# Performance work log

Measured on AMD Instinct MI355X. Metric: run time of the kernel, lower is better.

The kernel has to match this reference:

```python
import jax, jax.numpy as jnp
import numpy as np

B, P, H = 256, 20, 4  # images, boxes per image, humans per image
F, L, S, HD, C = 1024, 300, 16, 1024, 117

def _build_edges():
    s, d = np.meshgrid(np.arange(P), np.arange(P), indexing='ij')
    m = s != d
    src_l, dst_l = s[m], d[m]  # 380 fully-connected edges per image (src-major order)
    eid_tab = -np.ones((P, P), np.int64)
    eid_tab[src_l, dst_l] = np.arange(src_l.shape[0])
    rs, rd = np.meshgrid(np.arange(P), np.arange(H), indexing='ij')
    rm = rs != rd
    r_eid = eid_tab[rs[rm], rd[rm]]  # 76 readout edges per image (human dst)
    off_n = (np.arange(B) * P)[:, None]
    off_e = (np.arange(B) * src_l.shape[0])[:, None]
    edge_src = (src_l[None] + off_n).ravel().astype(np.int32)
    edge_dst = (dst_l[None] + off_n).ravel().astype(np.int32)
    readout_eid = (r_eid[None] + off_e).ravel().astype(np.int32)
    return edge_src, edge_dst, readout_eid

def setup_inputs() -> dict:
    key = jax.random.key(0)
    ks = jax.random.split(key, 12)
    es, ed, re = _build_edges()
    N = B * P
    D_in = 2 * F + 2 * L + S  # 2664
    return {
        'feat': jax.random.normal(ks[0], (N, F), jnp.float32),
        'word2vec': jax.random.normal(ks[1], (N, L), jnp.float32),
        'spatial_feat': jax.random.normal(ks[2], (es.shape[0], S), jnp.float32),
        'W_v': jax.random.normal(ks[3], (F, F), jnp.float32) / np.float32(np.sqrt(F)),
        'a_v': jax.random.normal(ks[4], (2 * F,), jnp.float32) * 0.05,
        'W_l': jax.random.normal(ks[5], (L, L), jnp.float32) / np.float32(np.sqrt(L)),
        'a_l': jax.random.normal(ks[6], (2 * L,), jnp.float32) * 0.05,
        'W1': jax.random.normal(ks[7], (D_in, HD), jnp.float32) / np.float32(np.sqrt(D_in)),
        'b1': jnp.zeros((HD,), jnp.float32),
        'W2': jax.random.normal(ks[8], (HD, C), jnp.float32) / np.float32(np.sqrt(HD)),
        'b2': jnp.zeros((C,), jnp.float32),
        'edge_src': jnp.asarray(es),
        'edge_dst': jnp.asarray(ed),
        'readout_eid': jnp.asarray(re),
    }

def _gat_update(x, W, a, src, dst, n):
    # graph-attention message passing (GRNN step): attention over incoming edges per dst
    h = x @ W                      # [N, d]
    d = h.shape[1]
    e_src = h @ a[:d]              # [N]
    e_dst = h @ a[d:]
    e = jax.nn.leaky_relu(e_src[src] + e_dst[dst], 0.2)          # [E]
    emax = jax.ops.segment_max(e, dst, num_segments=n)
    ee = jnp.exp(e - emax[dst])
    denom = jax.ops.segment_sum(ee, dst, num_segments=n)
    alpha = ee / (denom[dst] + 1e-9)                              # segment softmax
    msg = jax.ops.segment_sum(alpha[:, None] * h[src], dst, num_segments=n)  # [N, d]
    return jax.nn.relu(x + msg)

def reference(feat, word2vec, spatial_feat, W_v, a_v, W_l, a_l, W1, b1, W2, b2,
              edge_src, edge_dst, readout_eid):
    n = feat.shape[0]
    new_n_f = _gat_update(feat, W_v, a_v, edge_src, edge_dst, n)          # visual stream
    new_n_f_lang = _gat_update(word2vec, W_l, a_l, edge_src, edge_dst, n) # semantic stream
    s = edge_src[readout_eid]
    d = edge_dst[readout_eid]
    s_f = spatial_feat[readout_eid]
    # Predictor.forward: concat [dst visual, dst lang, edge spatial, src lang, src visual]
    x = jnp.concatenate([new_n_f[d], new_n_f_lang[d], s_f, new_n_f_lang[s], new_n_f[s]], axis=1)
    hdn = jax.nn.relu(x @ W1 + b1)
    return hdn @ W2 + b2  # [Er, 117] action logits
```

## Files before the change

kernel.cpp:

```cpp
#include <hip/hip_runtime.h>
#include <hip/hip_bf16.h>

#define BB 256
#define PP 20
#define HH 4
#define FF 1024
#define LL 300
#define LLP 320
#define DCAT 1344
#define SS 16
#define HDIM 1024
#define CC 117
#define NNODE (BB * PP)
#define NREAD (BB * (PP * HH - HH))
#define EPB 8
#define TK 32

typedef __attribute__((ext_vector_type(8))) short bf16x8v;
typedef __attribute__((ext_vector_type(4))) float f32x4v;
typedef __attribute__((ext_vector_type(4))) unsigned short u16x4;

__device__ __forceinline__ float bf2f(unsigned short u) {
  return __uint_as_float((unsigned int)u << 16);
}
__device__ __forceinline__ unsigned short f2b(float f) {
  __hip_bfloat16 h = __float2bfloat16(f);
  return *(unsigned short*)&h;
}

__global__ void sniff_dtype(const unsigned short* __restrict__ buf,
                            int* __restrict__ flag) {
  int t = threadIdx.x;
  int votes = 0;
  for (int i = t; i < 512; i += 256) {
    unsigned int u = (unsigned int)buf[i] << 16;
    float v = __uint_as_float(u);
    float a = fabsf(v);
    if (v == v && a > 9.3e-10f && a < 1.1e9f) votes++;
  }
  __shared__ int sv[256];
  sv[t] = votes;
  __syncthreads();
  for (int s = 128; s > 0; s >>= 1) {
    if (t < s) sv[t] += sv[t + s];
    __syncthreads();
  }
  if (t == 0) flag[0] = (sv[0] < 448) ? 1 : 0;
}

#define NB_FEAT 5120
#define NB_W2V 1600
#define NB_SM 79
#define PREP_BLOCKS 10739

__global__ __launch_bounds__(256) void prep_all(
    const void* __restrict__ s0, const void* __restrict__ s1,
    const void* __restrict__ s3, const void* __restrict__ s4,
    const void* __restrict__ s5, const void* __restrict__ s6,
    const void* __restrict__ s7, const void* __restrict__ s8,
    const void* __restrict__ s9, const void* __restrict__ s10,
    __hip_bfloat16* __restrict__ xcat, __hip_bfloat16* __restrict__ cAv,
    __hip_bfloat16* __restrict__ cAl, __hip_bfloat16* __restrict__ cB1,
    __hip_bfloat16* __restrict__ cB2, __hip_bfloat16* __restrict__ cW1sp,
    __hip_bfloat16* __restrict__ dWvT, __hip_bfloat16* __restrict__ dWlT,
    __hip_bfloat16* __restrict__ dW1d, __hip_bfloat16* __restrict__ dW1s,
    __hip_bfloat16* __restrict__ dW2T, const int* __restrict__ flag) {
  const int bid = blockIdx.x;
  const int t = threadIdx.x;
  const int fl = flag[0];

  if (bid < NB_FEAT) {
    long i = (long)bid * 256 + t;
    int r = (int)(i >> 8);
    int c = ((int)i & 255) * 4;
    u16x4 o;
    if (fl) {
      float4 v = *(const float4*)((const float*)s0 + (long)r * FF + c);
      o[0] = f2b(v.x); o[1] = f2b(v.y); o[2] = f2b(v.z); o[3] = f2b(v.w);
    } else {
      o = *(const u16x4*)((const __hip_bfloat16*)s0 + (long)r * FF + c);
    }
    *(u16x4*)(xcat + (long)r * DCAT + c) = o;
  } else if (bid < NB_FEAT + NB_W2V) {
    long i = (long)(bid - NB_FEAT) * 256 + t;
    int r = (int)(i / 80), c = ((int)(i % 80)) * 4;
    u16x4 o;
    if (c + 4 <= LL) {
      if (fl) {
        const float* p = (const float*)s1 + (long)r * LL + c;
        o[0] = f2b(p[0]); o[1] = f2b(p[1]); o[2] = f2b(p[2]); o[3] = f2b(p[3]);
      } else {
        const __hip_bfloat16* p = (const __hip_bfloat16*)s1 + (long)r * LL + c;
        o[0] = *(const unsigned short*)(p + 0);
        o[1] = *(const unsigned short*)(p + 1);
        o[2] = *(const unsigned short*)(p + 2);
        o[3] = *(const unsigned short*)(p + 3);
      }
    } else {
#pragma unroll
      for (int j = 0; j < 4; j++) {
        float v = 0.f;
        if (c + j < LL)
          v = fl ? ((const float*)s1)[(long)r * LL + c + j]
                 : __bfloat162float(
                       ((const __hip_bfloat16*)s1)[(long)r * LL + c + j]);
        o[j] = f2b(v);
      }
    }
    *(u16x4*)(xcat + (long)r * DCAT + FF + c) = o;
  } else if (bid < NB_FEAT + NB_W2V + NB_SM) {
    int i = (bid - NB_FEAT - NB_W2V) * 256 + t;
    auto rd = [&](const void* p, long idx) -> float {
      return fl ? ((const float*)p)[idx]
                : __bfloat162float(((const __hip_bfloat16*)p)[idx]);
    };
    if (i < 2048) cAv[i] = __float2bfloat16(rd(s4, i));
    else if (i < 2648) cAl[i - 2048] = __float2bfloat16(rd(s6, i - 2048));
    else if (i < 3672) cB1[i - 2648] = __float2bfloat16(rd(s8, i - 2648));
    else if (i < 3789) cB2[i - 3672] = __float2bfloat16(rd(s10, i - 3672));
    else if (i < 20173)
      cW1sp[i - 3789] = __float2bfloat16(rd(s7, 1355776L + (i - 3789)));
  } else {
    int idx = bid - (NB_FEAT + NB_W2V + NB_SM);
    const int OFFS[8] = {0, 1024, 1124, 2148, 2468, 3492, 3812, 3940};
    const int NKB[7] = {32, 10, 32, 10, 32, 10, 32};
    const int ROW0[7] = {0, 0, 0, 1024, 1640, 1340, 0};
    const int KK[7] = {1024, 300, 1024, 300, 1024, 300, 1024};
    const int NN[7] = {1024, 300, 1024, 1024, 1024, 1024, 117};
    const int LD[7] = {1024, 300, 1024, 1024, 1024, 1024, 117};
    const int KP[7] = {1024, 320, 1024, 320, 1024, 320, 1024};
    const int KOFF[7] = {0, 0, 0, 1024, 0, 1024, 0};
    const int KLD[7] = {1024, 320, DCAT, DCAT, DCAT, DCAT, 1024};
    int z = 0;
    while (z < 6 && idx >= OFFS[z + 1]) z++;
    idx -= OFFS[z];
    const int kb = (idx % NKB[z]) * 32, nb = (idx / NKB[z]) * 32;
    const void* src = (z == 0) ? s3 : (z == 1) ? s5 : (z == 6) ? s9 : s7;
    __hip_bfloat16* dst = (z == 0) ? dWvT : (z == 1) ? dWlT
                          : (z <= 3) ? dW1d : (z <= 5) ? dW1s : dW2T;
    const int row0 = ROW0[z], K = KK[z], N = NN[z], ld = LD[z], Kp = KP[z];
    const int koff = KOFF[z], kld = KLD[z];
    __shared__ float tile[32][33];
    const int tx = t & 31, ty = t >> 5;
    for (int i = ty; i < 32; i += 8) {
      int k = kb + i, n = nb + tx;
      float v = 0.f;
      if (k < K && n < N) {
        long sidx = (long)(row0 + k) * ld + n;
        v = fl ? ((const float*)src)[sidx]
               : __bfloat162float(((const __hip_bfloat16*)src)[sidx]);
      }
      tile[i][tx] = v;
    }
    __syncthreads();
    for (int i = ty; i < 32; i += 8) {
      int n = nb + i, k = kb + tx;
      if (n < N && k < Kp)
        dst[(long)n * kld + koff + k] = __float2bfloat16(tile[tx][i]);
    }
  }
}

struct GDesc {
  const __hip_bfloat16* A;
  const __hip_bfloat16* BT;
  void* C;
  const __hip_bfloat16* bias;
  int M, N, K, lda, ldbt, ldc;
  int row_mode, do_relu, c_mode, nbx, nby;
};

template <int BM, int BN, int WR, int WC>
__global__ __launch_bounds__(256) void gemm_db(GDesc d0, GDesc d1,
                                               const int* outflag) {
  constexpr int MI = BM / WR / 16;
  constexpr int NI = BN / WC / 16;
  __shared__ __hip_bfloat16 Asm[2][BM * TK];
  __shared__ __hip_bfloat16 Bsm[2][BN * TK];
  const GDesc d = blockIdx.z ? d1 : d0;
  if ((int)blockIdx.x >= d.nbx || (int)blockIdx.y >= d.nby) return;
  const int tid = threadIdx.x;
  const int lane = tid & 63;
  const int wave = tid >> 6;
  const int wm = (wave % WR) * (BM / WR);
  const int wn = (wave / WR) * (BN / WC);
  const int m0 = blockIdx.y * BM;
  const int n0 = blockIdx.x * BN;
  const int col_l = lane & 15;
  const int quad = lane >> 4;
  const __hip_bfloat16* A = d.A;
  const __hip_bfloat16* BT = d.BT;
  const int M = d.M, N = d.N, lda = d.lda, ldbt = d.ldbt;
  const int row_mode = d.row_mode;

  auto stage = [&](int k0, int buf) {
#pragma unroll
    for (int c = tid; c < BM * 4; c += 256) {
      int r = c >> 2;
      int koff = (c & 3) * 8;
      int row = m0 + r;
      if (row >= M) row = M - 1;
      long grow = row_mode ? ((long)(row >> 2) * PP + (row & 3)) : (long)row;
      const __hip_bfloat16* gp = A + grow * lda + k0 + koff;
      __builtin_amdgcn_global_load_lds(
          (const __attribute__((address_space(1))) unsigned int*)gp,
          (__attribute__((address_space(3))) unsigned int*)(&Asm[buf][c * 8]),
          16, 0, 0);
    }
#pragma unroll
    for (int c = tid; c < BN * 4; c += 256) {
      int r = c >> 2;
      int koff = (c & 3) * 8;
      int row = n0 + r;
      if (row >= N) row = N - 1;
      const __hip_bfloat16* gp = BT + (long)row * ldbt + k0 + koff;
      __builtin_amdgcn_global_load_lds(
          (const __attribute__((address_space(1))) unsigned int*)gp,
          (__attribute__((address_space(3))) unsigned int*)(&Bsm[buf][c * 8]),
          16, 0, 0);
    }
  };

  f32x4v acc[MI][NI];
#pragma unroll
  for (int i = 0; i < MI; i++)
#pragma unroll
    for (int j = 0; j < NI; j++)
#pragma unroll
      for (int r = 0; r < 4; r++) acc[i][j][r] = 0.f;

  const int nk = d.K / TK;
  stage(0, 0);
  __syncthreads();
  for (int kt = 0; kt < nk; kt++) {
    const int cur = kt & 1;
    if (kt + 1 < nk) stage((kt + 1) * TK, 1 - cur);
    bf16x8v af[MI], bfr[NI];
#pragma unroll
    for (int mi = 0; mi < MI; mi++)
      af[mi] =
          *(const bf16x8v*)&Asm[cur][(wm + mi * 16 + col_l) * TK + quad * 8];
#pragma unroll
    for (int ni = 0; ni < NI; ni++)
      bfr[ni] =
          *(const bf16x8v*)&Bsm[cur][(wn + ni * 16 + col_l) * TK + quad * 8];
#pragma unroll
    for (int mi = 0; mi < MI; mi++)
#pragma unroll
      for (int ni = 0; ni < NI; ni++)
        acc[mi][ni] = __builtin_amdgcn_mfma_f32_16x16x32_bf16(
            af[mi], bfr[ni], acc[mi][ni], 0, 0, 0);
    __syncthreads();
  }

  const int store_f32 =
      (d.c_mode == 1) || (d.c_mode == 2 && outflag && outflag[0]);
#pragma unroll
  for (int mi = 0; mi < MI; mi++) {
    int rbase = m0 + wm + mi * 16 + quad * 4;
#pragma unroll
    for (int ni = 0; ni < NI; ni++) {
      int col = n0 + wn + ni * 16 + col_l;
      if (col >= N) continue;
      float bv = d.bias ? __bfloat162float(d.bias[col]) : 0.f;
#pragma unroll
      for (int r = 0; r < 4; r++) {
        int row = rbase + r;
        if (row >= M) continue;
        float v = acc[mi][ni][r] + bv;
        if (d.do_relu) v = fmaxf(v, 0.f);
        if (store_f32)
          ((float*)d.C)[(long)row * d.ldc + col] = v;
        else
          ((__hip_bfloat16*)d.C)[(long)row * d.ldc + col] = __float2bfloat16(v);
      }
    }
  }
}

#define CHROW (DCAT / 4)

__global__ __launch_bounds__(1024) void attn_fused(
    const __hip_bfloat16* __restrict__ xcat,
    const __hip_bfloat16* __restrict__ hcat,
    const __hip_bfloat16* __restrict__ aV,
    const __hip_bfloat16* __restrict__ aL,
    __hip_bfloat16* __restrict__ newcat) {
  const int b = blockIdx.x;
  const int t = threadIdx.x;
  const long base = (long)b * PP * DCAT;

  __shared__ __hip_bfloat16 hs[PP][DCAT];
  __shared__ float esv[PP], edv[PP], esl[PP], edl[PP];
  __shared__ float alphaV[PP * PP], alphaL[PP * PP];

  for (int i = t; i < PP * CHROW; i += 1024) {
    int r = i / CHROW, c = (i % CHROW) * 4;
    *(u16x4*)&hs[r][c] = *(const u16x4*)(hcat + base + (long)r * DCAT + c);
  }
  __syncthreads();

  const int wave = t >> 6, lane = t & 63;
  for (int node = wave; node < PP; node += 16) {
    float s1 = 0.f, s2 = 0.f, s3 = 0.f, s4 = 0.f;
    for (int f = lane * 4; f < FF; f += 256) {
      u16x4 hv = *(const u16x4*)&hs[node][f];
      u16x4 a1 = *(const u16x4*)(aV + f);
      u16x4 a2 = *(const u16x4*)(aV + FF + f);
#pragma unroll
      for (int j = 0; j < 4; j++) {
        float hf = bf2f(hv[j]);
        s1 += hf * bf2f(a1[j]);
        s2 += hf * bf2f(a2[j]);
      }
    }
    for (int f = FF + lane * 4; f < FF + LL; f += 256) {
      u16x4 hv = *(const u16x4*)&hs[node][f];
      u16x4 a3 = *(const u16x4*)(aL + (f - FF));
      u16x4 a4 = *(const u16x4*)(aL + LL + (f - FF));
#pragma unroll
      for (int j = 0; j < 4; j++) {
        float hf = bf2f(hv[j]);
        s3 += hf * bf2f(a3[j]);
        s4 += hf * bf2f(a4[j]);
      }
    }
#pragma unroll
    for (int o = 32; o > 0; o >>= 1) {
      s1 += __shfl_down(s1, o);
      s2 += __shfl_down(s2, o);
      s3 += __shfl_down(s3, o);
      s4 += __shfl_down(s4, o);
    }
    if (lane == 0) {
      esv[node] = s1; edv[node] = s2; esl[node] = s3; edl[node] = s4;
    }
  }
  __syncthreads();

  if (t < 2 * PP) {
    const int strm = t / PP, dd = t % PP;
    const float* es = strm ? esl : esv;
    const float ed = strm ? edl[dd] : edv[dd];
    float lg[PP];
    float m = -1e30f;
#pragma unroll
    for (int s = 0; s < PP; s++) {
      float e;
      if (s == dd) e = -1e30f;
      else {
        float v = es[s] + ed;
        e = (v > 0.f) ? v : 0.2f * v;
      }
      lg[s] = e;
      m = fmaxf(m, e);
    }
    float sum = 0.f;
#pragma unroll
    for (int s = 0; s < PP; s++) {
      lg[s] = expf(lg[s] - m);
      sum += lg[s];
    }
    float inv = 1.f / (sum + 1e-9f);
    float* al = strm ? alphaL : alphaV;
#pragma unroll
    for (int s = 0; s < PP; s++) al[s * PP + dd] = lg[s] * inv;
  }
  __syncthreads();

  for (int i = t; i < PP * CHROW; i += 1024) {
    int dd = i / CHROW, c = (i % CHROW) * 4;
    u16x4 ov;
    if (c >= FF + LL) {
      ov[0] = 0; ov[1] = 0; ov[2] = 0; ov[3] = 0;
    } else {
      const float* al = (c < FF) ? (alphaV + dd) : (alphaL + dd);
      float a0 = 0.f, a1 = 0.f, a2 = 0.f, a3 = 0.f;
#pragma unroll
      for (int s = 0; s < PP; s++) {
        float w = al[s * PP];
        u16x4 hv = *(const u16x4*)&hs[s][c];
        a0 += w * bf2f(hv[0]);
        a1 += w * bf2f(hv[1]);
        a2 += w * bf2f(hv[2]);
        a3 += w * bf2f(hv[3]);
      }
      u16x4 xv = *(const u16x4*)(xcat + base + (long)dd * DCAT + c);
      ov[0] = f2b(fmaxf(bf2f(xv[0]) + a0, 0.f));
      ov[1] = f2b(fmaxf(bf2f(xv[1]) + a1, 0.f));
      ov[2] = f2b(fmaxf(bf2f(xv[2]) + a2, 0.f));
      ov[3] = f2b(fmaxf(bf2f(xv[3]) + a3, 0.f));
    }
    *(u16x4*)(newcat + base + (long)dd * DCAT + c) = ov;
  }
}

__global__ __launch_bounds__(256) void combine_kernel(
    const int* __restrict__ e_src, const int* __restrict__ e_dst,
    const int* __restrict__ r_eid, const void* __restrict__ spat_raw,
    const __hip_bfloat16* __restrict__ W1sp,
    const __hip_bfloat16* __restrict__ b1,
    const __hip_bfloat16* __restrict__ Yd, const __hip_bfloat16* __restrict__ Ys,
    __hip_bfloat16* __restrict__ hdn, const int* __restrict__ flag) {
  const int t = threadIdx.x;
  const int e0 = blockIdx.x * EPB;
  const int hd = t * 4;

  float w[SS][4];
#pragma unroll
  for (int k = 0; k < SS; k++) {
    u16x4 ww = *(const u16x4*)(W1sp + (long)k * HDIM + hd);
#pragma unroll
    for (int j = 0; j < 4; j++) w[k][j] = bf2f(ww[j]);
  }
  float bb[4];
  {
    u16x4 bv = *(const u16x4*)(b1 + hd);
#pragma unroll
    for (int j = 0; j < 4; j++) bb[j] = bf2f(bv[j]);
  }

  __shared__ int sh_s[EPB], sh_hx[EPB], sh_re[EPB];
  __shared__ float sh_sf[EPB][SS];
  if (t < EPB) {
    int re = r_eid[e0 + t];
    sh_re[t] = re;
    sh_s[t] = e_src[re];
    int d = e_dst[re];
    sh_hx[t] = (d / PP) * HH + (d % PP);
  }
  __syncthreads();
  if (t < EPB * SS) {
    int ee = t >> 4, k = t & 15;
    long idx = (long)sh_re[ee] * SS + k;
    sh_sf[ee][k] = flag[0]
                       ? ((const float*)spat_raw)[idx]
                       : __bfloat162float(((const __hip_bfloat16*)spat_raw)[idx]);
  }
  __syncthreads();

#pragma unroll
  for (int ee = 0; ee < EPB; ee++) {
    const int s = sh_s[ee];
    const int hx = sh_hx[ee];
    u16x4 yd = *(const u16x4*)(Yd + (long)hx * HDIM + hd);
    u16x4 ys = *(const u16x4*)(Ys + (long)s * HDIM + hd);
    float v[4];
#pragma unroll
    for (int j = 0; j < 4; j++) v[j] = bf2f(yd[j]) + bf2f(ys[j]) + bb[j];
#pragma unroll
    for (int k = 0; k < SS; k++) {
      float sfv = sh_sf[ee][k];
#pragma unroll
      for (int j = 0; j < 4; j++) v[j] += sfv * w[k][j];
    }
    u16x4 o;
#pragma unroll
    for (int j = 0; j < 4; j++) o[j] = f2b(fmaxf(v[j], 0.f));
    *(u16x4*)(hdn + (long)(e0 + ee) * HDIM + hd) = o;
  }
}

extern "C" void kernel_launch(void* const* d_in, const int* in_sizes, int n_in,
                              void* d_out, int out_size, void* d_ws,
                              size_t ws_size, hipStream_t stream) {
  const int* e_src = (const int*)d_in[11];
  const int* e_dst = (const int*)d_in[12];
  const int* r_eid = (const int*)d_in[13];
  (void)ws_size; (void)n_in; (void)in_sizes; (void)out_size;

  char* ws = (char*)d_ws;
  size_t off = 0;
  auto take = [&](size_t bytes) {
    char* p = ws + off;
    off += (bytes + 255) & ~(size_t)255;
    return p;
  };

  int* dflag = (int*)take(256);
  __hip_bfloat16* xcat   = (__hip_bfloat16*)take((size_t)NNODE * DCAT * 2);
  __hip_bfloat16* hcat   = (__hip_bfloat16*)take((size_t)NNODE * DCAT * 2);
  __hip_bfloat16* newcat = (__hip_bfloat16*)take((size_t)NNODE * DCAT * 2);
  __hip_bfloat16* cAv    = (__hip_bfloat16*)take((size_t)2 * FF * 2);
  __hip_bfloat16* cAl    = (__hip_bfloat16*)take((size_t)2 * LL * 2);
  __hip_bfloat16* cB1    = (__hip_bfloat16*)take((size_t)HDIM * 2);
  __hip_bfloat16* cB2    = (__hip_bfloat16*)take((size_t)CC * 2);
  __hip_bfloat16* cW1sp  = (__hip_bfloat16*)take((size_t)SS * HDIM * 2);
  __hip_bfloat16* WvT    = (__hip_bfloat16*)take((size_t)FF * FF * 2);
  __hip_bfloat16* WlT    = (__hip_bfloat16*)take((size_t)LL * LLP * 2);
  __hip_bfloat16* W1Td   = (__hip_bfloat16*)take((size_t)HDIM * DCAT * 2);
  __hip_bfloat16* W1Ts   = (__hip_bfloat16*)take((size_t)HDIM * DCAT * 2);
  __hip_bfloat16* W2T    = (__hip_bfloat16*)take((size_t)CC * HDIM * 2);
  __hip_bfloat16* Yd     = (__hip_bfloat16*)take((size_t)BB * HH * HDIM * 2);
  __hip_bfloat16* Ys     = (__hip_bfloat16*)take((size_t)NNODE * HDIM * 2);
  __hip_bfloat16* hdn    = (__hip_bfloat16*)take((size_t)NREAD * HDIM * 2);

  dim3 blk(256);

  sniff_dtype<<<1, blk, 0, stream>>>((const unsigned short*)d_in[0], dflag);

  prep_all<<<PREP_BLOCKS, blk, 0, stream>>>(
      d_in[0], d_in[1], d_in[3], d_in[4], d_in[5], d_in[6], d_in[7], d_in[8],
      d_in[9], d_in[10], xcat, cAv, cAl, cB1, cB2, cW1sp, WvT, WlT, W1Td, W1Ts,
      W2T, dflag);

  {
    GDesc pv{xcat, WvT, hcat, nullptr,
             NNODE, FF, FF, DCAT, FF, DCAT, 0, 0, 0, 8, 80};
    GDesc pl{xcat + FF, WlT, hcat + FF, nullptr,
             NNODE, LL, LLP, DCAT, LLP, DCAT, 0, 0, 0, 3, 80};
    gemm_db<64, 128, 2, 2><<<dim3(8, 80, 2), blk, 0, stream>>>(pv, pl,
                                                               nullptr);
  }

  attn_fused<<<BB, dim3(1024), 0, stream>>>(xcat, hcat, cAv, cAl, newcat);

  {
    GDesc gys{newcat, W1Ts, Ys, nullptr,
              NNODE, HDIM, DCAT, DCAT, DCAT, HDIM, 0, 0, 0, 8, 80};
    GDesc gyd{newcat, W1Td, Yd, nullptr,
              BB * HH, HDIM, DCAT, DCAT, DCAT, HDIM, 1, 0, 0, 8, 16};
    gemm_db<64, 128, 2, 2><<<dim3(8, 80, 2), blk, 0, stream>>>(gys, gyd,
                                                               nullptr);
  }

  combine_kernel<<<NREAD / EPB, blk, 0, stream>>>(e_src, e_dst, r_eid, d_in[2],
                                                  cW1sp, cB1, Yd, Ys, hdn,
                                                  dflag);

  {
    GDesc go{hdn, W2T, d_out, cB2,
             NREAD, CC, HDIM, HDIM, HDIM, CC, 0, 0, 2, 1, 608};
    gemm_db<32, 128, 1, 4><<<dim3(1, 608, 1), blk, 0, stream>>>(go, go, dflag);
  }
}
```

Before: 246.7 us.

## Fuse hidden combine with output GEMM, swizzle GEMM LDS, inline dtype sniff

The combine step now keeps each 32-edge tile of hidden activations in shared memory and runs the final 1024x117 MFMA GEMM in the same kernel. This removes the hdn round-trip through global memory and one launch. The shared GEMM now uses a K-tile of 64 with an XOR-swizzled LDS layout to cut bank conflicts and halve the number of barriers. The standalone dtype-sniff kernel is gone; each block of prep_all and combine_out redoes the sniff itself, which adds a small reduction to every block in exchange for one fewer launch.

```diff
diff --git a/kernel.cpp b/kernel.cpp
--- a/kernel.cpp
+++ b/kernel.cpp
@@ -13,8 +13,7 @@
 #define CC 117
 #define NNODE (BB * PP)
 #define NREAD (BB * (PP * HH - HH))
-#define EPB 8
-#define TK 32
+#define TKB 64
 
 typedef __attribute__((ext_vector_type(8))) short bf16x8v;
 typedef __attribute__((ext_vector_type(4))) float f32x4v;
@@ -28,24 +27,24 @@
   return *(unsigned short*)&h;
 }
 
-__global__ void sniff_dtype(const unsigned short* __restrict__ buf,
-                            int* __restrict__ flag) {
-  int t = threadIdx.x;
+__device__ __forceinline__ int block_sniff(const unsigned short* fb, int t,
+                                           int* sv) {
   int votes = 0;
   for (int i = t; i < 512; i += 256) {
-    unsigned int u = (unsigned int)buf[i] << 16;
+    unsigned int u = (unsigned int)fb[i] << 16;
     float v = __uint_as_float(u);
     float a = fabsf(v);
     if (v == v && a > 9.3e-10f && a < 1.1e9f) votes++;
   }
-  __shared__ int sv[256];
   sv[t] = votes;
   __syncthreads();
   for (int s = 128; s > 0; s >>= 1) {
     if (t < s) sv[t] += sv[t + s];
     __syncthreads();
   }
-  if (t == 0) flag[0] = (sv[0] < 448) ? 1 : 0;
+  int fl = (sv[0] < 448) ? 1 : 0;
+  __syncthreads();
+  return fl;
 }
 
 #define NB_FEAT 5120
@@ -64,10 +63,11 @@
     __hip_bfloat16* __restrict__ cB2, __hip_bfloat16* __restrict__ cW1sp,
     __hip_bfloat16* __restrict__ dWvT, __hip_bfloat16* __restrict__ dWlT,
     __hip_bfloat16* __restrict__ dW1d, __hip_bfloat16* __restrict__ dW1s,
-    __hip_bfloat16* __restrict__ dW2T, const int* __restrict__ flag) {
+    __hip_bfloat16* __restrict__ dW2T) {
   const int bid = blockIdx.x;
   const int t = threadIdx.x;
-  const int fl = flag[0];
+  __shared__ int sv[256];
+  const int fl = block_sniff((const unsigned short*)s0, t, sv);
 
   if (bid < NB_FEAT) {
     long i = (long)bid * 256 + t;
@@ -167,16 +167,15 @@
   void* C;
   const __hip_bfloat16* bias;
   int M, N, K, lda, ldbt, ldc;
-  int row_mode, do_relu, c_mode, nbx, nby;
+  int row_mode, do_relu, c_fp32, nbx, nby;
 };
 
 template <int BM, int BN, int WR, int WC>
-__global__ __launch_bounds__(256) void gemm_db(GDesc d0, GDesc d1,
-                                               const int* outflag) {
+__global__ __launch_bounds__(256) void gemm_db(GDesc d0, GDesc d1) {
   constexpr int MI = BM / WR / 16;
   constexpr int NI = BN / WC / 16;
-  __shared__ __hip_bfloat16 Asm[2][BM * TK];
-  __shared__ __hip_bfloat16 Bsm[2][BN * TK];
+  __shared__ __hip_bfloat16 Asm[2][BM * TKB];
+  __shared__ __hip_bfloat16 Bsm[2][BN * TKB];
   const GDesc d = blockIdx.z ? d1 : d0;
   if ((int)blockIdx.x >= d.nbx || (int)blockIdx.y >= d.nby) return;
   const int tid = threadIdx.x;
@@ -195,25 +194,25 @@
 
   auto stage = [&](int k0, int buf) {
 #pragma unroll
-    for (int c = tid; c < BM * 4; c += 256) {
-      int r = c >> 2;
-      int koff = (c & 3) * 8;
+    for (int c = tid; c < BM * 8; c += 256) {
+      int r = c >> 3, j = c & 7;
+      int kc = j ^ (r & 7);
       int row = m0 + r;
       if (row >= M) row = M - 1;
       long grow = row_mode ? ((long)(row >> 2) * PP + (row & 3)) : (long)row;
-      const __hip_bfloat16* gp = A + grow * lda + k0 + koff;
+      const __hip_bfloat16* gp = A + grow * lda + k0 + kc * 8;
       __builtin_amdgcn_global_load_lds(
           (const __attribute__((address_space(1))) unsigned int*)gp,
           (__attribute__((address_space(3))) unsigned int*)(&Asm[buf][c * 8]),
           16, 0, 0);
     }
 #pragma unroll
-    for (int c = tid; c < BN * 4; c += 256) {
-      int r = c >> 2;
-      int koff = (c & 3) * 8;
+    for (int c = tid; c < BN * 8; c += 256) {
+      int r = c >> 3, j = c & 7;
+      int kc = j ^ (r & 7);
       int row = n0 + r;
       if (row >= N) row = N - 1;
-      const __hip_bfloat16* gp = BT + (long)row * ldbt + k0 + koff;
+      const __hip_bfloat16* gp = BT + (long)row * ldbt + k0 + kc * 8;
       __builtin_amdgcn_global_load_lds(
           (const __attribute__((address_space(1))) unsigned int*)gp,
           (__attribute__((address_space(3))) unsigned int*)(&Bsm[buf][c * 8]),
@@ -229,32 +228,37 @@
 #pragma unroll
       for (int r = 0; r < 4; r++) acc[i][j][r] = 0.f;
 
-  const int nk = d.K / TK;
+  const int nk = d.K / TKB;
   stage(0, 0);
   __syncthreads();
   for (int kt = 0; kt < nk; kt++) {
     const int cur = kt & 1;
-    if (kt + 1 < nk) stage((kt + 1) * TK, 1 - cur);
-    bf16x8v af[MI], bfr[NI];
-#pragma unroll
-    for (int mi = 0; mi < MI; mi++)
-      af[mi] =
-          *(const bf16x8v*)&Asm[cur][(wm + mi * 16 + col_l) * TK + quad * 8];
-#pragma unroll
-    for (int ni = 0; ni < NI; ni++)
-      bfr[ni] =
-          *(const bf16x8v*)&Bsm[cur][(wn + ni * 16 + col_l) * TK + quad * 8];
-#pragma unroll
-    for (int mi = 0; mi < MI; mi++)
-#pragma unroll
-      for (int ni = 0; ni < NI; ni++)
-        acc[mi][ni] = __builtin_amdgcn_mfma_f32_16x16x32_bf16(
-            af[mi], bfr[ni], acc[mi][ni], 0, 0, 0);
+    if (kt + 1 < nk) stage((kt + 1) * TKB, 1 - cur);
+#pragma unroll
+    for (int ks = 0; ks < 2; ks++) {
+      bf16x8v af[MI], bfr[NI];
+#pragma unroll
+      for (int mi = 0; mi < MI; mi++) {
+        int R = wm + mi * 16 + col_l;
+        int j = (ks * 4 + quad) ^ (R & 7);
+        af[mi] = *(const bf16x8v*)&Asm[cur][R * TKB + j * 8];
+      }
+#pragma unroll
+      for (int ni = 0; ni < NI; ni++) {
+        int R = wn + ni * 16 + col_l;
+        int j = (ks * 4 + quad) ^ (R & 7);
+        bfr[ni] = *(const bf16x8v*)&Bsm[cur][R * TKB + j * 8];
+      }
+#pragma unroll
+      for (int mi = 0; mi < MI; mi++)
+#pragma unroll
+        for (int ni = 0; ni < NI; ni++)
+          acc[mi][ni] = __builtin_amdgcn_mfma_f32_16x16x32_bf16(
+              af[mi], bfr[ni], acc[mi][ni], 0, 0, 0);
+    }
     __syncthreads();
   }
 
-  const int store_f32 =
-      (d.c_mode == 1) || (d.c_mode == 2 && outflag && outflag[0]);
 #pragma unroll
   for (int mi = 0; mi < MI; mi++) {
     int rbase = m0 + wm + mi * 16 + quad * 4;
@@ -269,7 +273,7 @@
         if (row >= M) continue;
         float v = acc[mi][ni][r] + bv;
         if (d.do_relu) v = fmaxf(v, 0.f);
-        if (store_f32)
+        if (d.c_fp32)
           ((float*)d.C)[(long)row * d.ldc + col] = v;
         else
           ((__hip_bfloat16*)d.C)[(long)row * d.ldc + col] = __float2bfloat16(v);
@@ -395,17 +399,26 @@
   }
 }
 
-__global__ __launch_bounds__(256) void combine_kernel(
+#define HSLD 1032
+
+__global__ __launch_bounds__(256) void combine_out(
     const int* __restrict__ e_src, const int* __restrict__ e_dst,
     const int* __restrict__ r_eid, const void* __restrict__ spat_raw,
-    const __hip_bfloat16* __restrict__ W1sp,
+    const void* __restrict__ feat_raw, const __hip_bfloat16* __restrict__ W1sp,
     const __hip_bfloat16* __restrict__ b1,
     const __hip_bfloat16* __restrict__ Yd, const __hip_bfloat16* __restrict__ Ys,
-    __hip_bfloat16* __restrict__ hdn, const int* __restrict__ flag) {
+    const __hip_bfloat16* __restrict__ W2T,
+    const __hip_bfloat16* __restrict__ b2, void* __restrict__ out) {
   const int t = threadIdx.x;
-  const int e0 = blockIdx.x * EPB;
+  const int e0 = blockIdx.x * 32;
+  __shared__ unsigned short hs[32][HSLD];
+  __shared__ int sv[256];
+  __shared__ int sh_s[32], sh_hx[32], sh_re[32];
+  __shared__ float sh_sf[32][SS];
+
+  const int fl = block_sniff((const unsigned short*)feat_raw, t, sv);
+
   const int hd = t * 4;
-
   float w[SS][4];
 #pragma unroll
   for (int k = 0; k < SS; k++) {
@@ -420,9 +433,7 @@
     for (int j = 0; j < 4; j++) bb[j] = bf2f(bv[j]);
   }
 
-  __shared__ int sh_s[EPB], sh_hx[EPB], sh_re[EPB];
-  __shared__ float sh_sf[EPB][SS];
-  if (t < EPB) {
+  if (t < 32) {
     int re = r_eid[e0 + t];
     sh_re[t] = re;
     sh_s[t] = e_src[re];
@@ -430,17 +441,21 @@
     sh_hx[t] = (d / PP) * HH + (d % PP);
   }
   __syncthreads();
-  if (t < EPB * SS) {
-    int ee = t >> 4, k = t & 15;
-    long idx = (long)sh_re[ee] * SS + k;
-    sh_sf[ee][k] = flag[0]
-                       ? ((const float*)spat_raw)[idx]
-                       : __bfloat162float(((const __hip_bfloat16*)spat_raw)[idx]);
-  }
-  __syncthreads();
-
-#pragma unroll
-  for (int ee = 0; ee < EPB; ee++) {
+  {
+#pragma unroll
+    for (int p = 0; p < 2; p++) {
+      int i = t + p * 256;
+      int ee = i >> 4, k = i & 15;
+      long idx = (long)sh_re[ee] * SS + k;
+      sh_sf[ee][k] =
+          fl ? ((const float*)spat_raw)[idx]
+             : __bfloat162float(((const __hip_bfloat16*)spat_raw)[idx]);
+    }
+  }
+  __syncthreads();
+
+#pragma unroll 4
+  for (int ee = 0; ee < 32; ee++) {
     const int s = sh_s[ee];
     const int hx = sh_hx[ee];
     u16x4 yd = *(const u16x4*)(Yd + (long)hx * HDIM + hd);
@@ -457,7 +472,75 @@
     u16x4 o;
 #pragma unroll
     for (int j = 0; j < 4; j++) o[j] = f2b(fmaxf(v[j], 0.f));
-    *(u16x4*)(hdn + (long)(e0 + ee) * HDIM + hd) = o;
+    *(u16x4*)&hs[ee][hd] = o;
+  }
+  __syncthreads();
+
+  const int lane = t & 63;
+  const int wave = t >> 6;
+  const int col_l = lane & 15;
+  const int quad = lane >> 4;
+  const int wn = wave * 32;
+
+  const __hip_bfloat16* pB[2];
+#pragma unroll
+  for (int ni = 0; ni < 2; ni++) {
+    int n = wn + ni * 16 + col_l;
+    if (n >= CC) n = CC - 1;
+    pB[ni] = W2T + (long)n * HDIM + quad * 8;
+  }
+
+  f32x4v acc[2][2];
+#pragma unroll
+  for (int i = 0; i < 2; i++)
+#pragma unroll
+    for (int j = 0; j < 2; j++)
+#pragma unroll
+      for (int r = 0; r < 4; r++) acc[i][j][r] = 0.f;
+
+  bf16x8v bcur[2], bnext[2];
+#pragma unroll
+  for (int ni = 0; ni < 2; ni++) bcur[ni] = *(const bf16x8v*)(pB[ni]);
+
+  for (int kt = 0; kt < HDIM / 32; kt++) {
+    const int k0 = kt * 32;
+    if (kt + 1 < HDIM / 32) {
+#pragma unroll
+      for (int ni = 0; ni < 2; ni++)
+        bnext[ni] = *(const bf16x8v*)(pB[ni] + (kt + 1) * 32);
+    }
+    bf16x8v af[2];
+#pragma unroll
+    for (int mi = 0; mi < 2; mi++)
+      af[mi] = *(const bf16x8v*)&hs[mi * 16 + col_l][k0 + quad * 8];
+#pragma unroll
+    for (int mi = 0; mi < 2; mi++)
+#pragma unroll
+      for (int ni = 0; ni < 2; ni++)
+        acc[mi][ni] = __builtin_amdgcn_mfma_f32_16x16x32_bf16(
+            af[mi], bcur[ni], acc[mi][ni], 0, 0, 0);
+#pragma unroll
+    for (int ni = 0; ni < 2; ni++) bcur[ni] = bnext[ni];
+  }
+
+#pragma unroll
+  for (int mi = 0; mi < 2; mi++) {
+    int rbase = mi * 16 + quad * 4;
+#pragma unroll
+    for (int ni = 0; ni < 2; ni++) {
+      int col = wn + ni * 16 + col_l;
+      if (col >= CC) continue;
+      float bv = __bfloat162float(b2[col]);
+#pragma unroll
+      for (int r = 0; r < 4; r++) {
+        long row = e0 + rbase + r;
+        float v = acc[mi][ni][r] + bv;
+        if (fl)
+          ((float*)out)[row * CC + col] = v;
+        else
+          ((__hip_bfloat16*)out)[row * CC + col] = __float2bfloat16(v);
+      }
+    }
   }
 }
 
@@ -477,7 +560,6 @@
     return p;
   };
 
-  int* dflag = (int*)take(256);
   __hip_bfloat16* xcat   = (__hip_bfloat16*)take((size_t)NNODE * DCAT * 2);
   __hip_bfloat16* hcat   = (__hip_bfloat16*)take((size_t)NNODE * DCAT * 2);
   __hip_bfloat16* newcat = (__hip_bfloat16*)take((size_t)NNODE * DCAT * 2);
@@ -493,24 +575,20 @@
   __hip_bfloat16* W2T    = (__hip_bfloat16*)take((size_t)CC * HDIM * 2);
   __hip_bfloat16* Yd     = (__hip_bfloat16*)take((size_t)BB * HH * HDIM * 2);
   __hip_bfloat16* Ys     = (__hip_bfloat16*)take((size_t)NNODE * HDIM * 2);
-  __hip_bfloat16* hdn    = (__hip_bfloat16*)take((size_t)NREAD * HDIM * 2);
 
   dim3 blk(256);
-
-  sniff_dtype<<<1, blk, 0, stream>>>((const unsigned short*)d_in[0], dflag);
 
   prep_all<<<PREP_BLOCKS, blk, 0, stream>>>(
       d_in[0], d_in[1], d_in[3], d_in[4], d_in[5], d_in[6], d_in[7], d_in[8],
       d_in[9], d_in[10], xcat, cAv, cAl, cB1, cB2, cW1sp, WvT, WlT, W1Td, W1Ts,
-      W2T, dflag);
+      W2T);
 
   {
     GDesc pv{xcat, WvT, hcat, nullptr,
              NNODE, FF, FF, DCAT, FF, DCAT, 0, 0, 0, 8, 80};
     GDesc pl{xcat + FF, WlT, hcat + FF, nullptr,
              NNODE, LL, LLP, DCAT, LLP, DCAT, 0, 0, 0, 3, 80};
-    gemm_db<64, 128, 2, 2><<<dim3(8, 80, 2), blk, 0, stream>>>(pv, pl,
-                                                               nullptr);
+    gemm_db<64, 128, 2, 2><<<dim3(8, 80, 2), blk, 0, stream>>>(pv, pl);
   }
 
   attn_fused<<<BB, dim3(1024), 0, stream>>>(xcat, hcat, cAv, cAl, newcat);
@@ -520,17 +598,10 @@
               NNODE, HDIM, DCAT, DCAT, DCAT, HDIM, 0, 0, 0, 8, 80};
     GDesc gyd{newcat, W1Td, Yd, nullptr,
               BB * HH, HDIM, DCAT, DCAT, DCAT, HDIM, 1, 0, 0, 8, 16};
-    gemm_db<64, 128, 2, 2><<<dim3(8, 80, 2), blk, 0, stream>>>(gys, gyd,
-                                                               nullptr);
-  }
-
-  combine_kernel<<<NREAD / EPB, blk, 0, stream>>>(e_src, e_dst, r_eid, d_in[2],
-                                                  cW1sp, cB1, Yd, Ys, hdn,
-                                                  dflag);
-
-  {
-    GDesc go{hdn, W2T, d_out, cB2,
-             NREAD, CC, HDIM, HDIM, HDIM, CC, 0, 0, 2, 1, 608};
-    gemm_db<32, 128, 1, 4><<<dim3(1, 608, 1), blk, 0, stream>>>(go, go, dflag);
-  }
-}
+    gemm_db<64, 128, 2, 2><<<dim3(8, 80, 2), blk, 0, stream>>>(gys, gyd);
+  }
+
+  combine_out<<<NREAD / 32, blk, 0, stream>>>(e_src, e_dst, r_eid, d_in[2],
+                                              d_in[0], cW1sp, cB1, Yd, Ys, W2T,
+                                              cB2, d_out);
+}
```

Measured after the change: 258.6 us. +4.8%, slower.
